# Kernel optimization log

Measured on AMD Instinct MI355X. Metric: run time of the kernel, lower is better.

Reference implementation:

```python
import jax, jax.numpy as jnp
import numpy as np
from jax import lax

H = 64      # hidden_size
VOC = 512   # num_embedding
L = 2       # num_layers


def layernorm(x, g, b, eps=1e-5):
    mu = jnp.mean(x, axis=-1, keepdims=True)
    var = jnp.mean((x - mu) ** 2, axis=-1, keepdims=True)
    return (x - mu) * lax.rsqrt(var + eps) * g + b


def conv3d(x, w, b):
    # x: [B, U, V, W, Cin] (channels-last), w: [3,3,3,Cin,Cout]
    return lax.conv_general_dilated(
        x, w, (1, 1, 1), 'SAME',
        dimension_numbers=('NDHWC', 'DHWIO', 'NDHWC')) + b


def setup_inputs() -> dict:
    key = jax.random.key(0)
    ks = jax.random.split(key, 8)
    f = lambda k, s, sc: jax.random.normal(k, s, jnp.float32) * sc
    return {
        'code': jax.random.randint(ks[0], (2, 5, 1, 8, 8, 8), 0, VOC),
        'ncode': jax.random.randint(ks[1], (2, 3, 1, 8, 8, 8), 0, VOC),
        'emb': f(ks[2], (VOC, H), 0.02),
        'win': f(ks[3], (L, 3, 3, 3, H, 4 * H), 0.05),
        'bin_': jnp.zeros((L, 4 * H), jnp.float32),
        'gin_w': jnp.ones((L, 4 * H), jnp.float32),
        'gin_b': jnp.zeros((L, 4 * H), jnp.float32),
        'wh': f(ks[4], (L, 3, 3, 3, H, 4 * H), 0.05),
        'bh': jnp.zeros((L, 4 * H), jnp.float32),
        'gh_w': jnp.ones((L, 4 * H), jnp.float32),
        'gh_b': jnp.zeros((L, 4 * H), jnp.float32),
        'w1': f(ks[5], (H, H), 0.05),
        'b1': jnp.zeros((H,), jnp.float32),
        'ln_g': jnp.ones((H,), jnp.float32),
        'ln_b': jnp.zeros((H,), jnp.float32),
        'w2': f(ks[6], (H, VOC), 0.05),
        'b2': jnp.zeros((VOC,), jnp.float32),
    }


def _forward(code, ncode, emb, win, bin_, gin_w, gin_b, wh, bh, gh_w, gh_b,
             w1, b1, ln_g, ln_b, w2, b2):
    N, Sn, C, U, V, W = ncode.shape
    x = jnp.concatenate([code, ncode[:, :-1]], axis=1)  # [N,S,C,U,V,W]
    S = x.shape[1]
    x = jnp.transpose(x, (0, 2, 1, 3, 4, 5)).reshape(N * C, S, U, V, W)
    h = emb[x]  # [NC, S, U, V, W, H]
    Hd = h.shape[-1]
    for i in range(L):
        # input-path conv is recurrence-free: batch it over all timesteps
        gi = layernorm(conv3d(h.reshape(N * C * S, U, V, W, Hd), win[i], bin_[i]),
                       gin_w[i], gin_b[i])
        gi = jnp.moveaxis(gi.reshape(N * C, S, U, V, W, 4 * Hd), 1, 0)  # [S,NC,U,V,W,4H]

        def step(carry, g, i=i):
            hx, cx = carry
            gates = g + layernorm(conv3d(hx, wh[i], bh[i]), gh_w[i], gh_b[i])
            ig, fg, cg, og = jnp.split(gates, 4, axis=-1)
            cx = jax.nn.sigmoid(fg) * cx + jax.nn.sigmoid(ig) * jnp.tanh(cg)
            hx = jax.nn.sigmoid(og) * jnp.tanh(cx)
            return (hx, cx), hx

        z = jnp.zeros((N * C, U, V, W, Hd), h.dtype)
        _, ys = lax.scan(step, (z, z), gi)
        h = jnp.moveaxis(ys, 0, 1)  # [NC,S,U,V,W,H]
    h = h[:, -Sn:].reshape(N, C, Sn, U, V, W, Hd)
    h = jnp.transpose(h, (0, 2, 1, 3, 4, 5, 6))  # [N,Sn,C,U,V,W,H]
    z = jax.nn.gelu(layernorm(h @ w1 + b1, ln_g, ln_b), approximate=False)
    logits = z @ w2 + b2  # [N,Sn,C,U,V,W,VOC]
    score = jnp.transpose(logits, (0, 6, 1, 2, 3, 4, 5))  # [N,VOC,Sn,C,U,V,W]
    logp = jax.nn.log_softmax(logits, axis=-1)
    loss = -jnp.mean(jnp.take_along_axis(logp, ncode[..., None], axis=-1))
    pred = jnp.argmax(score, axis=1)
    return score, loss, pred


def reference(code, ncode, emb, win, bin_, gin_w, gin_b, wh, bh, gh_w, gh_b,
              w1, b1, ln_g, ln_b, w2, b2):
    return _forward(code, ncode, emb, win, bin_, gin_w, gin_b, wh, bh,
                    gh_w, gh_b, w1, b1, ln_g, ln_b, w2, b2)
```

## Files before the change

### kernel.cpp

```cpp
#include <hip/hip_runtime.h>


typedef _Float16 f16;
typedef _Float16 f16x8 __attribute__((ext_vector_type(8)));
typedef float    f32x4 __attribute__((ext_vector_type(4)));

#define WSTRIDE 442368
#define WPT     884736
#define XSP     65536
#define HSP     458752

__device__ __forceinline__ float wred_sum(float v) {
    #pragma unroll
    for (int o = 32; o > 0; o >>= 1) v += __shfl_down(v, o, 64);
    return __shfl(v, 0, 64);
}
__device__ __forceinline__ float fsig(float x)  { return 1.f / (1.f + __expf(-x)); }
__device__ __forceinline__ float ftanh(float x) { return 1.f - 2.f / (__expf(2.f*x) + 1.f); }

__global__ __launch_bounds__(256) void embed_kernel(
    const int* __restrict__ code, const int* __restrict__ ncode,
    const float* __restrict__ emb, f16* __restrict__ h)
{
    int e = blockIdx.x * 256 + threadIdx.x;
    int ch = e & 63;
    int pos = e >> 6;
    int vox = pos & 511;
    int t = pos >> 9;
    int s = t % 7, nc = t / 7;
    int tok = (s < 5) ? code[(nc*5 + s)*512 + vox]
                      : ncode[(nc*3 + (s-5))*512 + vox];
    float x = emb[tok*64 + ch];
    f16 hi = (f16)x;
    h[(size_t)pos*128 + ch]      = hi;
    h[(size_t)pos*128 + 64 + ch] = (f16)(x - (float)hi);
}

__global__ __launch_bounds__(256) void wsplit_kernel(
    const float* __restrict__ win, const float* __restrict__ wh,
    f16* __restrict__ wp)
{
    int b = blockIdx.x;
    int tensor = b / 27, tap = b % 27;
    const float* src = ((tensor & 1) ? wh : win) + (tensor >> 1) * WSTRIDE
                     + tap * 16384;
    int co = threadIdx.x;
    int sw = co & 7;
    f16* dst = wp + ((size_t)(tensor*27 + tap)*256 + co) * 128;
    #pragma unroll
    for (int c8 = 0; c8 < 8; ++c8) {
        f16x8 hi8, lo8;
        #pragma unroll
        for (int j = 0; j < 8; ++j) {
            float w = src[(c8*8 + j)*256 + co] * 64.f;
            f16 hv = (f16)w;
            hi8[j] = hv;
            lo8[j] = (f16)(w - (float)hv);
        }
        *(f16x8*)(dst + ((c8 ^ sw)    )*8) = hi8;
        *(f16x8*)(dst + ((c8 ^ sw) + 8)*8) = lo8;
    }
}

struct MJob { const f16* x; const f16* w; const float* bias; float* y; };
struct MJobs { MJob j[4]; };

__global__ __launch_bounds__(256, 1) void conv_mfma_kernel(MJobs js)
{
    const MJob J = js.j[blockIdx.y];
    __shared__ float4 smem[4096];
    f16* wbuf = (f16*)smem;

    const int bx = blockIdx.x;
    const int slab = bx >> 5, u = (bx >> 2) & 7, cog = bx & 3;
    const int t = threadIdx.x, wid = t >> 6, l = t & 63;
    const int lv = (l >> 3) & 1, lw = l & 7, khi = l >> 4;

    const f16* xbase = J.x + (size_t)slab * HSP;
    const f16* wjob  = J.w + (size_t)cog * 8192;
    f16* wmine = wbuf + wid * 8192;

    const int t0 = wid * 7;
    const int ntap = (wid == 3) ? 6 : 7;

    f16x8 wreg[16];
    auto wload = [&](int tap) {
        const f16* src = wjob + (size_t)tap * 32768 + l * 8;
        #pragma unroll
        for (int i = 0; i < 16; ++i) wreg[i] = *(const f16x8*)(src + i * 512);
    };
    auto wstore = [&]() {
        f16* dst = wmine + l * 8;
        #pragma unroll
        for (int i = 0; i < 16; ++i) *(f16x8*)(dst + i * 512) = wreg[i];
    };

    wload(t0); wstore();

    f32x4 acc[4][4] = {};
    for (int tt = 0; tt < ntap; ++tt) {
        const int tap = t0 + tt;
        if (tt + 1 < ntap) wload(tap + 1);
        const int du = tap / 9, rr = tap % 9, dv = rr / 3, dw = rr % 3;
        const int uu = u + du - 1;
        const bool uok = (unsigned)uu < 8u;
        const f16* xrow[4]; bool ok[4];
        #pragma unroll
        for (int a = 0; a < 4; ++a) {
            int vs = a*2 + lv + dv - 1, ws = lw + dw - 1;
            ok[a] = uok && (unsigned)vs < 8u && (unsigned)ws < 8u;
            xrow[a] = xbase + ((size_t)(uu*64 + vs*8 + ws) << 7) + khi*8;
        }
        const f16* wrow = wmine + (l & 15) * 128;
        #pragma unroll
        for (int hs = 0; hs < 2; ++hs) {
            const int sc = ((hs*4 + khi) ^ lw) * 8;
            f16x8 ahi[4], alo[4], bhi[4], blo[4];
            #pragma unroll
            for (int a = 0; a < 4; ++a) {
                f16x8 v = {0,0,0,0,0,0,0,0}, v2 = v;
                if (ok[a]) {
                    v  = *(const f16x8*)(xrow[a] + hs*32);
                    v2 = *(const f16x8*)(xrow[a] + 64 + hs*32);
                }
                ahi[a] = v; alo[a] = v2;
            }
            #pragma unroll
            for (int n = 0; n < 4; ++n) {
                bhi[n] = *(const f16x8*)(wrow + n*2048 + sc);
                blo[n] = *(const f16x8*)(wrow + n*2048 + 64 + sc);
            }
            #pragma unroll
            for (int a = 0; a < 4; ++a)
                #pragma unroll
                for (int n = 0; n < 4; ++n)
                    acc[a][n] = __builtin_amdgcn_mfma_f32_16x16x32_f16(
                        ahi[a], bhi[n], acc[a][n], 0, 0, 0);
            #pragma unroll
            for (int a = 0; a < 4; ++a)
                #pragma unroll
                for (int n = 0; n < 4; ++n)
                    acc[a][n] = __builtin_amdgcn_mfma_f32_16x16x32_f16(
                        alo[a], bhi[n], acc[a][n], 0, 0, 0);
            #pragma unroll
            for (int a = 0; a < 4; ++a)
                #pragma unroll
                for (int n = 0; n < 4; ++n)
                    acc[a][n] = __builtin_amdgcn_mfma_f32_16x16x32_f16(
                        ahi[a], blo[n], acc[a][n], 0, 0, 0);
        }
        if (tt + 1 < ntap) wstore();
    }

    f32x4* red = (f32x4*)smem;
    {
        f32x4* mine = red + (size_t)(wid * 64 + l) * 16;
        #pragma unroll
        for (int a = 0; a < 4; ++a)
            #pragma unroll
            for (int n = 0; n < 4; ++n)
                mine[(a * 4 + n) ^ (l & 15)] = acc[a][n];
    }
    __syncthreads();
    {
        const int a = t >> 6, ll = t & 63;
        #pragma unroll
        for (int n = 0; n < 4; ++n) {
            const int ch = (a * 4 + n) ^ (ll & 15);
            f32x4 sv = red[(0 * 64 + ll) * 16 + ch]
                     + red[(1 * 64 + ll) * 16 + ch]
                     + red[(2 * 64 + ll) * 16 + ch]
                     + red[(3 * 64 + ll) * 16 + ch];
            const int co = cog * 64 + n * 16 + (ll & 15);
            const float bvv = J.bias[co];
            #pragma unroll
            for (int r = 0; r < 4; ++r) {
                int vox = a * 16 + (ll >> 4) * 4 + r;
                J.y[(size_t)(slab * 512 + u * 64 + vox) * 256 + co]
                    = sv[r] * 0.015625f + bvv;
            }
        }
    }
}

struct GJob {
    const float* giraw; const float* ghat;
    const float* ginw; const float* ginb;
    const float* ghw;  const float* ghb;
    float* cx; f16* h16; int k; int k0;
};
__global__ __launch_bounds__(256) void gates_step_kernel(GJob ja, GJob jb)
{
    const GJob J = (blockIdx.y == 0) ? ja : jb;
    const int wid = threadIdx.x >> 6, lane = threadIdx.x & 63;
    const int row = blockIdx.x * 4 + wid;
    const int nc = row >> 9, vox = row & 511;

    const float* g1 = J.giraw + (size_t)row*256;
    float a0 = g1[lane], a1 = g1[64+lane], a2 = g1[128+lane], a3 = g1[192+lane];
    float mu1 = wred_sum(a0+a1+a2+a3) * (1.f/256.f);
    float d0=a0-mu1, d1=a1-mu1, d2=a2-mu1, d3=a3-mu1;
    float v1 = wred_sum(d0*d0+d1*d1+d2*d2+d3*d3) * (1.f/256.f);
    float rs1 = rsqrtf(v1 + 1e-5f);

    const float* g2 = J.k0 ? J.ghat : J.ghat + (size_t)row*256;
    float b0 = g2[lane], b1 = g2[64+lane], b2 = g2[128+lane], b3 = g2[192+lane];
    float mu2 = wred_sum(b0+b1+b2+b3) * (1.f/256.f);
    float e0=b0-mu2, e1=b1-mu2, e2=b2-mu2, e3=b3-mu2;
    float v2 = wred_sum(e0*e0+e1*e1+e2*e2+e3*e3) * (1.f/256.f);
    float rs2 = rsqrtf(v2 + 1e-5f);

    float Ig = d0*rs1*J.ginw[lane]     + J.ginb[lane]     + e0*rs2*J.ghw[lane]     + J.ghb[lane];
    float Fg = d1*rs1*J.ginw[64+lane]  + J.ginb[64+lane]  + e1*rs2*J.ghw[64+lane]  + J.ghb[64+lane];
    float Cg = d2*rs1*J.ginw[128+lane] + J.ginb[128+lane] + e2*rs2*J.ghw[128+lane] + J.ghb[128+lane];
    float Og = d3*rs1*J.ginw[192+lane] + J.ginb[192+lane] + e3*rs2*J.ghw[192+lane] + J.ghb[192+lane];

    float c_old = J.k0 ? 0.f : J.cx[(size_t)row*64 + lane];
    float c_new = fsig(Fg)*c_old + fsig(Ig)*ftanh(Cg);
    float h_new = fsig(Og)*ftanh(c_new);
    J.cx[(size_t)row*64 + lane] = c_new;
    size_t hb = ((size_t)(nc*7 + J.k)*512 + vox)*128 + lane;
    f16 hi = (f16)h_new;
    J.h16[hb]      = hi;
    J.h16[hb + 64] = (f16)(h_new - (float)hi);
}

__global__ __launch_bounds__(256) void head_kernel(
    const f16* __restrict__ h,
    const float* __restrict__ w1, const float* __restrict__ b1,
    const float* __restrict__ lng, const float* __restrict__ lnb,
    const float* __restrict__ w2, const float* __restrict__ b2,
    const int* __restrict__ ncode,
    float* __restrict__ out)
{
    __shared__ float zv[4][64];
    __shared__ float lg[4][512];
    const int blk = blockIdx.x;
    const int n = blk / 384;
    const int sn = (blk / 128) % 3;
    const int vox0 = (blk & 127) * 4;
    const int wid = threadIdx.x >> 6, lane = threadIdx.x & 63;
    const int vox = vox0 + wid;
    const int r = (n*3 + sn)*512 + vox;
    const f16* hv = h + (size_t)((n*7 + sn + 4)*512 + vox)*128;

    float yv = b1[lane];
    for (int kk = 0; kk < 64; ++kk) {
        float hk = (float)hv[kk] + (float)hv[64 + kk];
        yv = fmaf(hk, w1[kk*64 + lane], yv);
    }
    float mu = wred_sum(yv) * (1.f/64.f);
    float d = yv - mu;
    float var = wred_sum(d*d) * (1.f/64.f);
    float ln = d * rsqrtf(var + 1e-5f) * lng[lane] + lnb[lane];
    zv[wid][lane] = 0.5f * ln * (1.f + erff(ln * 0.70710678118654752f));

    float l[8];
    #pragma unroll
    for (int j = 0; j < 8; ++j) l[j] = b2[j*64 + lane];
    for (int kk = 0; kk < 64; ++kk) {
        float zz = zv[wid][kk];
        #pragma unroll
        for (int j = 0; j < 8; ++j)
            l[j] = fmaf(zz, w2[kk*512 + j*64 + lane], l[j]);
    }
    #pragma unroll
    for (int j = 0; j < 8; ++j) lg[wid][j*64 + lane] = l[j];

    float m = l[0]; int mi = lane;
    #pragma unroll
    for (int j = 1; j < 8; ++j)
        if (l[j] > m) { m = l[j]; mi = j*64 + lane; }
    #pragma unroll
    for (int o = 32; o > 0; o >>= 1) {
        float om = __shfl_down(m, o, 64);
        int   oi = __shfl_down(mi, o, 64);
        if (om > m || (om == m && oi < mi)) { m = om; mi = oi; }
    }
    float maxv = __shfl(m, 0, 64);
    int   maxi = __shfl(mi, 0, 64);
    float es = 0.f;
    #pragma unroll
    for (int j = 0; j < 8; ++j) es += __expf(l[j] - maxv);
    float sum = wred_sum(es);
    if (lane == 0) {
        int target = ncode[(n*3 + sn)*512 + vox];
        float logp = lg[wid][target] - maxv - __logf(sum);
        atomicAdd(out + 1572864, -logp * (1.f/3072.f));
        out[1572865 + r] = (float)maxi;
    }

    __syncthreads();
    const int t = threadIdx.x;
    #pragma unroll
    for (int jj = 0; jj < 2; ++jj) {
        int co = t + jj*256;
        float4 o4 = { lg[0][co], lg[1][co], lg[2][co], lg[3][co] };
        *(float4*)(out + (size_t)((n*512 + co)*3 + sn)*512 + vox0) = o4;
    }
}

extern "C" void kernel_launch(void* const* d_in, const int* in_sizes, int n_in,
                              void* d_out, int out_size, void* d_ws, size_t ws_size,
                              hipStream_t stream) {
    (void)in_sizes; (void)n_in; (void)out_size; (void)ws_size;
    const int*   code  = (const int*)d_in[0];
    const int*   ncode = (const int*)d_in[1];
    const float* emb   = (const float*)d_in[2];
    const float* win   = (const float*)d_in[3];
    const float* bin_  = (const float*)d_in[4];
    const float* gin_w = (const float*)d_in[5];
    const float* gin_b = (const float*)d_in[6];
    const float* wh    = (const float*)d_in[7];
    const float* bh    = (const float*)d_in[8];
    const float* gh_w  = (const float*)d_in[9];
    const float* gh_b  = (const float*)d_in[10];
    const float* w1    = (const float*)d_in[11];
    const float* b1    = (const float*)d_in[12];
    const float* ln_g  = (const float*)d_in[13];
    const float* ln_b  = (const float*)d_in[14];
    const float* w2    = (const float*)d_in[15];
    const float* b2    = (const float*)d_in[16];
    float* out = (float*)d_out;

    float* base  = (float*)d_ws;
    f16*   wp    = (f16*)base;
    f16*   h1    = (f16*)(base + 1769472);
    f16*   h2    = h1 + 917504;
    float* gi1   = base + 2686976;
    float* gi2   = gi1 + 262144;
    float* ghat1 = gi2 + 262144;
    float* ghat2 = ghat1 + 262144;
    float* cx1   = ghat2 + 262144;
    float* cx2   = cx1 + 65536;

    const f16* win0 = wp;
    const f16* wh0  = wp + WPT;
    const f16* win1 = wp + 2*WPT;
    const f16* wh1  = wp + 3*WPT;

    hipMemsetAsync(out + 1572864, 0, sizeof(float), stream);
    embed_kernel<<<1792, 256, 0, stream>>>(code, ncode, emb, h1);
    wsplit_kernel<<<108, 256, 0, stream>>>(win, wh, wp);

    {
        MJobs js{};
        js.j[0] = { h1, win0, bin_, gi1 };
        conv_mfma_kernel<<<dim3(64, 1), 256, 0, stream>>>(js);
    }

    for (int s = 0; s <= 7; ++s) {
        GJob g1 = { gi1, (s == 0) ? bh : ghat1,
                    gin_w, gin_b, gh_w, gh_b, cx1, h1, s, s == 0 };
        GJob g2 = { gi2, (s == 1) ? bh + 256 : ghat2,
                    gin_w + 256, gin_b + 256, gh_w + 256, gh_b + 256,
                    cx2, h2, s - 1, s == 1 };
        if (s == 0)
            gates_step_kernel<<<dim3(256, 1), 256, 0, stream>>>(g1, g1);
        else if (s <= 6)
            gates_step_kernel<<<dim3(256, 2), 256, 0, stream>>>(g1, g2);
        else
            gates_step_kernel<<<dim3(256, 1), 256, 0, stream>>>(g2, g2);

        MJobs js{}; int nj = 0;
        if (s <= 5) js.j[nj++] = { h1 + (size_t)(s+1)*XSP, win0, bin_,     gi1 };
        if (s <= 5) js.j[nj++] = { h1 + (size_t)s*XSP,     wh0,  bh,       ghat1 };
        if (s <= 6) js.j[nj++] = { h1 + (size_t)s*XSP,     win1, bin_+256, gi2 };
        if (s >= 1 && s <= 6)
                    js.j[nj++] = { h2 + (size_t)(s-1)*XSP, wh1,  bh+256,   ghat2 };
        if (nj > 0)
            conv_mfma_kernel<<<dim3(64, nj), 256, 0, stream>>>(js);
    }

    head_kernel<<<768, 256, 0, stream>>>(h2, w1, b1, ln_g, ln_b, w2, b2, ncode, out);
}
```

Measured before the change: 335.0 us.

## Split conv K-dimension across two blocks and batch head over 16 voxels

Result: no change. 336.0 us (+0.3%).

```diff
diff --git a/kernel.cpp b/kernel.cpp
--- a/kernel.cpp
+++ b/kernel.cpp
@@ -9,6 +9,7 @@
 #define WPT     884736
 #define XSP     65536
 #define HSP     458752
+#define GPART   262144
 
 __device__ __forceinline__ float wred_sum(float v) {
     #pragma unroll
@@ -46,61 +47,67 @@
                      + tap * 16384;
     int co = threadIdx.x;
     int sw = co & 7;
-    f16* dst = wp + ((size_t)(tensor*27 + tap)*256 + co) * 128;
-    #pragma unroll
-    for (int c8 = 0; c8 < 8; ++c8) {
-        f16x8 hi8, lo8;
-        #pragma unroll
-        for (int j = 0; j < 8; ++j) {
-            float w = src[(c8*8 + j)*256 + co] * 64.f;
-            f16 hv = (f16)w;
-            hi8[j] = hv;
-            lo8[j] = (f16)(w - (float)hv);
-        }
-        *(f16x8*)(dst + ((c8 ^ sw)    )*8) = hi8;
-        *(f16x8*)(dst + ((c8 ^ sw) + 8)*8) = lo8;
-    }
-}
-
-struct MJob { const f16* x; const f16* w; const float* bias; float* y; };
+    #pragma unroll
+    for (int hs = 0; hs < 2; ++hs) {
+        f16* dst = wp + (((size_t)tensor*27 + tap)*2 + hs)*16384 + co*64;
+        #pragma unroll
+        for (int j = 0; j < 4; ++j) {
+            f16x8 hi8, lo8;
+            #pragma unroll
+            for (int m = 0; m < 8; ++m) {
+                float w = src[(hs*32 + j*8 + m)*256 + co] * 64.f;
+                f16 hv = (f16)w;
+                hi8[m] = hv;
+                lo8[m] = (f16)(w - (float)hv);
+            }
+            *(f16x8*)(dst + ((j     ^ sw))*8) = hi8;
+            *(f16x8*)(dst + (((4+j) ^ sw))*8) = lo8;
+        }
+    }
+}
+
+struct MJob { const f16* x; const f16* w; float* y; };
 struct MJobs { MJob j[4]; };
 
-__global__ __launch_bounds__(256, 1) void conv_mfma_kernel(MJobs js)
+__global__ __launch_bounds__(256, 2) void conv_mfma_kernel(MJobs js)
 {
     const MJob J = js.j[blockIdx.y];
     __shared__ float4 smem[4096];
     f16* wbuf = (f16*)smem;
 
     const int bx = blockIdx.x;
-    const int slab = bx >> 5, u = (bx >> 2) & 7, cog = bx & 3;
+    const int cog = bx & 3, u = (bx >> 2) & 7, slab = (bx >> 5) & 1, kb = bx >> 6;
     const int t = threadIdx.x, wid = t >> 6, l = t & 63;
     const int lv = (l >> 3) & 1, lw = l & 7, khi = l >> 4;
 
+    const int gid = kb*4 + wid;
+    const int g0  = (gid < 6) ? gid*7 : 42 + (gid - 6)*6;
+    const int cnt = (gid < 6) ? 7 : 6;
+
     const f16* xbase = J.x + (size_t)slab * HSP;
-    const f16* wjob  = J.w + (size_t)cog * 8192;
+    const f16* wjob  = J.w + (size_t)cog * 4096;
     f16* wmine = wbuf + wid * 8192;
 
-    const int t0 = wid * 7;
-    const int ntap = (wid == 3) ? 6 : 7;
-
-    f16x8 wreg[16];
-    auto wload = [&](int tap) {
-        const f16* src = wjob + (size_t)tap * 32768 + l * 8;
-        #pragma unroll
-        for (int i = 0; i < 16; ++i) wreg[i] = *(const f16x8*)(src + i * 512);
+    f16x8 wreg[8];
+    auto wload = [&](int k) {
+        const f16* src = wjob + (size_t)k * 16384 + l * 8;
+        #pragma unroll
+        for (int i = 0; i < 8; ++i) wreg[i] = *(const f16x8*)(src + i * 512);
     };
-    auto wstore = [&]() {
-        f16* dst = wmine + l * 8;
-        #pragma unroll
-        for (int i = 0; i < 16; ++i) *(f16x8*)(dst + i * 512) = wreg[i];
+    auto wstore = [&](int b) {
+        f16* dst = wmine + b * 4096 + l * 8;
+        #pragma unroll
+        for (int i = 0; i < 8; ++i) *(f16x8*)(dst + i * 512) = wreg[i];
     };
 
-    wload(t0); wstore();
+    wload(g0); wstore(0);
 
     f32x4 acc[4][4] = {};
-    for (int tt = 0; tt < ntap; ++tt) {
-        const int tap = t0 + tt;
-        if (tt + 1 < ntap) wload(tap + 1);
+    int cur = 0;
+    for (int q = 0; q < cnt; ++q) {
+        const int k = g0 + q;
+        if (q + 1 < cnt) wload(k + 1);
+        const int tap = k >> 1, hs = k & 1;
         const int du = tap / 9, rr = tap % 9, dv = rr / 3, dw = rr % 3;
         const int uu = u + du - 1;
         const bool uok = (unsigned)uu < 8u;
@@ -111,45 +118,43 @@
             ok[a] = uok && (unsigned)vs < 8u && (unsigned)ws < 8u;
             xrow[a] = xbase + ((size_t)(uu*64 + vs*8 + ws) << 7) + khi*8;
         }
-        const f16* wrow = wmine + (l & 15) * 128;
-        #pragma unroll
-        for (int hs = 0; hs < 2; ++hs) {
-            const int sc = ((hs*4 + khi) ^ lw) * 8;
-            f16x8 ahi[4], alo[4], bhi[4], blo[4];
-            #pragma unroll
-            for (int a = 0; a < 4; ++a) {
-                f16x8 v = {0,0,0,0,0,0,0,0}, v2 = v;
-                if (ok[a]) {
-                    v  = *(const f16x8*)(xrow[a] + hs*32);
-                    v2 = *(const f16x8*)(xrow[a] + 64 + hs*32);
-                }
-                ahi[a] = v; alo[a] = v2;
+        const f16* wrow = wmine + cur*4096 + (l & 15)*64;
+        const int schi = ((khi    ) ^ lw) * 8;
+        const int sclo = ((4 + khi) ^ lw) * 8;
+        f16x8 ahi[4], alo[4], bhi[4], blo[4];
+        #pragma unroll
+        for (int a = 0; a < 4; ++a) {
+            f16x8 v = {0,0,0,0,0,0,0,0}, v2 = v;
+            if (ok[a]) {
+                v  = *(const f16x8*)(xrow[a] + hs*32);
+                v2 = *(const f16x8*)(xrow[a] + 64 + hs*32);
             }
-            #pragma unroll
-            for (int n = 0; n < 4; ++n) {
-                bhi[n] = *(const f16x8*)(wrow + n*2048 + sc);
-                blo[n] = *(const f16x8*)(wrow + n*2048 + 64 + sc);
-            }
-            #pragma unroll
-            for (int a = 0; a < 4; ++a)
-                #pragma unroll
-                for (int n = 0; n < 4; ++n)
-                    acc[a][n] = __builtin_amdgcn_mfma_f32_16x16x32_f16(
-                        ahi[a], bhi[n], acc[a][n], 0, 0, 0);
-            #pragma unroll
-            for (int a = 0; a < 4; ++a)
-                #pragma unroll
-                for (int n = 0; n < 4; ++n)
-                    acc[a][n] = __builtin_amdgcn_mfma_f32_16x16x32_f16(
-                        alo[a], bhi[n], acc[a][n], 0, 0, 0);
-            #pragma unroll
-            for (int a = 0; a < 4; ++a)
-                #pragma unroll
-                for (int n = 0; n < 4; ++n)
-                    acc[a][n] = __builtin_amdgcn_mfma_f32_16x16x32_f16(
-                        ahi[a], blo[n], acc[a][n], 0, 0, 0);
-        }
-        if (tt + 1 < ntap) wstore();
+            ahi[a] = v; alo[a] = v2;
+        }
+        #pragma unroll
+        for (int n = 0; n < 4; ++n) {
+            bhi[n] = *(const f16x8*)(wrow + n*1024 + schi);
+            blo[n] = *(const f16x8*)(wrow + n*1024 + sclo);
+        }
+        #pragma unroll
+        for (int a = 0; a < 4; ++a)
+            #pragma unroll
+            for (int n = 0; n < 4; ++n)
+                acc[a][n] = __builtin_amdgcn_mfma_f32_16x16x32_f16(
+                    ahi[a], bhi[n], acc[a][n], 0, 0, 0);
+        #pragma unroll
+        for (int a = 0; a < 4; ++a)
+            #pragma unroll
+            for (int n = 0; n < 4; ++n)
+                acc[a][n] = __builtin_amdgcn_mfma_f32_16x16x32_f16(
+                    alo[a], bhi[n], acc[a][n], 0, 0, 0);
+        #pragma unroll
+        for (int a = 0; a < 4; ++a)
+            #pragma unroll
+            for (int n = 0; n < 4; ++n)
+                acc[a][n] = __builtin_amdgcn_mfma_f32_16x16x32_f16(
+                    ahi[a], blo[n], acc[a][n], 0, 0, 0);
+        if (q + 1 < cnt) { wstore(cur ^ 1); cur ^= 1; }
     }
 
     f32x4* red = (f32x4*)smem;
@@ -163,6 +168,7 @@
     }
     __syncthreads();
     {
+        float* yp = J.y + (size_t)kb * GPART;
         const int a = t >> 6, ll = t & 63;
         #pragma unroll
         for (int n = 0; n < 4; ++n) {
@@ -172,19 +178,20 @@
                      + red[(2 * 64 + ll) * 16 + ch]
                      + red[(3 * 64 + ll) * 16 + ch];
             const int co = cog * 64 + n * 16 + (ll & 15);
-            const float bvv = J.bias[co];
             #pragma unroll
             for (int r = 0; r < 4; ++r) {
                 int vox = a * 16 + (ll >> 4) * 4 + r;
-                J.y[(size_t)(slab * 512 + u * 64 + vox) * 256 + co]
-                    = sv[r] * 0.015625f + bvv;
+                yp[(size_t)(slab * 512 + u * 64 + vox) * 256 + co]
+                    = sv[r] * 0.015625f;
             }
         }
     }
 }
 
 struct GJob {
-    const float* giraw; const float* ghat;
+    const float* giA; const float* giB;
+    const float* ghA; const float* ghB;
+    const float* bin; const float* bhb;
     const float* ginw; const float* ginb;
     const float* ghw;  const float* ghb;
     float* cx; f16* h16; int k; int k0;
@@ -196,15 +203,29 @@
     const int row = blockIdx.x * 4 + wid;
     const int nc = row >> 9, vox = row & 511;
 
-    const float* g1 = J.giraw + (size_t)row*256;
-    float a0 = g1[lane], a1 = g1[64+lane], a2 = g1[128+lane], a3 = g1[192+lane];
+    const float* gA = J.giA + (size_t)row*256;
+    const float* gB = J.giB + (size_t)row*256;
+    float a0 = gA[lane]     + gB[lane]     + J.bin[lane];
+    float a1 = gA[64+lane]  + gB[64+lane]  + J.bin[64+lane];
+    float a2 = gA[128+lane] + gB[128+lane] + J.bin[128+lane];
+    float a3 = gA[192+lane] + gB[192+lane] + J.bin[192+lane];
     float mu1 = wred_sum(a0+a1+a2+a3) * (1.f/256.f);
     float d0=a0-mu1, d1=a1-mu1, d2=a2-mu1, d3=a3-mu1;
     float v1 = wred_sum(d0*d0+d1*d1+d2*d2+d3*d3) * (1.f/256.f);
     float rs1 = rsqrtf(v1 + 1e-5f);
 
-    const float* g2 = J.k0 ? J.ghat : J.ghat + (size_t)row*256;
-    float b0 = g2[lane], b1 = g2[64+lane], b2 = g2[128+lane], b3 = g2[192+lane];
+    float b0, b1, b2, b3;
+    if (J.k0) {
+        b0 = J.bhb[lane]; b1 = J.bhb[64+lane];
+        b2 = J.bhb[128+lane]; b3 = J.bhb[192+lane];
+    } else {
+        const float* hA = J.ghA + (size_t)row*256;
+        const float* hB = J.ghB + (size_t)row*256;
+        b0 = hA[lane]     + hB[lane]     + J.bhb[lane];
+        b1 = hA[64+lane]  + hB[64+lane]  + J.bhb[64+lane];
+        b2 = hA[128+lane] + hB[128+lane] + J.bhb[128+lane];
+        b3 = hA[192+lane] + hB[192+lane] + J.bhb[192+lane];
+    }
     float mu2 = wred_sum(b0+b1+b2+b3) * (1.f/256.f);
     float e0=b0-mu2, e1=b1-mu2, e2=b2-mu2, e3=b3-mu2;
     float v2 = wred_sum(e0*e0+e1*e1+e2*e2+e3*e3) * (1.f/256.f);
@@ -233,70 +254,99 @@
     const int* __restrict__ ncode,
     float* __restrict__ out)
 {
-    __shared__ float zv[4][64];
-    __shared__ float lg[4][512];
+    __shared__ float hsm[16][64];
+    __shared__ float zv[16][64];
+    __shared__ float lg[10240];
     const int blk = blockIdx.x;
-    const int n = blk / 384;
-    const int sn = (blk / 128) % 3;
-    const int vox0 = (blk & 127) * 4;
-    const int wid = threadIdx.x >> 6, lane = threadIdx.x & 63;
-    const int vox = vox0 + wid;
-    const int r = (n*3 + sn)*512 + vox;
-    const f16* hv = h + (size_t)((n*7 + sn + 4)*512 + vox)*128;
-
-    float yv = b1[lane];
+    const int n = blk / 96;
+    const int sn = (blk / 32) % 3;
+    const int vox0 = (blk & 31) * 16;
+    const int t = threadIdx.x, wid = t >> 6, lane = t & 63;
+
+    for (int idx = t; idx < 1024; idx += 256) {
+        int vr = idx >> 6, ch = idx & 63;
+        const f16* hv = h + (size_t)((n*7 + sn + 4)*512 + vox0 + vr)*128;
+        hsm[vr][ch] = (float)hv[ch] + (float)hv[64 + ch];
+    }
+    __syncthreads();
+
+    float yva[4], yvb[4];
+    #pragma unroll
+    for (int r = 0; r < 4; ++r) { yva[r] = b1[lane]; yvb[r] = 0.f; }
+    for (int kk = 0; kk < 64; kk += 2) {
+        float w1a = w1[kk*64 + lane], w1b = w1[(kk+1)*64 + lane];
+        #pragma unroll
+        for (int r = 0; r < 4; ++r) {
+            yva[r] = fmaf(hsm[wid*4 + r][kk],     w1a, yva[r]);
+            yvb[r] = fmaf(hsm[wid*4 + r][kk + 1], w1b, yvb[r]);
+        }
+    }
+    #pragma unroll
+    for (int r = 0; r < 4; ++r) {
+        float yv = yva[r] + yvb[r];
+        float mu = wred_sum(yv) * (1.f/64.f);
+        float d = yv - mu;
+        float var = wred_sum(d*d) * (1.f/64.f);
+        float ln = d * rsqrtf(var + 1e-5f) * lng[lane] + lnb[lane];
+        zv[wid*4 + r][lane] = 0.5f * ln * (1.f + erff(ln * 0.70710678118654752f));
+    }
+    __syncthreads();
+
+    float l[4][8];
+    #pragma unroll
+    for (int r = 0; r < 4; ++r)
+        #pragma unroll
+        for (int j = 0; j < 8; ++j) l[r][j] = b2[j*64 + lane];
     for (int kk = 0; kk < 64; ++kk) {
-        float hk = (float)hv[kk] + (float)hv[64 + kk];
-        yv = fmaf(hk, w1[kk*64 + lane], yv);
-    }
-    float mu = wred_sum(yv) * (1.f/64.f);
-    float d = yv - mu;
-    float var = wred_sum(d*d) * (1.f/64.f);
-    float ln = d * rsqrtf(var + 1e-5f) * lng[lane] + lnb[lane];
-    zv[wid][lane] = 0.5f * ln * (1.f + erff(ln * 0.70710678118654752f));
-
-    float l[8];
-    #pragma unroll
-    for (int j = 0; j < 8; ++j) l[j] = b2[j*64 + lane];
-    for (int kk = 0; kk < 64; ++kk) {
-        float zz = zv[wid][kk];
+        float wv[8];
+        #pragma unroll
+        for (int j = 0; j < 8; ++j) wv[j] = w2[kk*512 + j*64 + lane];
+        #pragma unroll
+        for (int r = 0; r < 4; ++r) {
+            float zz = zv[wid*4 + r][kk];
+            #pragma unroll
+            for (int j = 0; j < 8; ++j) l[r][j] = fmaf(zz, wv[j], l[r][j]);
+        }
+    }
+    #pragma unroll
+    for (int r = 0; r < 4; ++r)
         #pragma unroll
         for (int j = 0; j < 8; ++j)
-            l[j] = fmaf(zz, w2[kk*512 + j*64 + lane], l[j]);
-    }
-    #pragma unroll
-    for (int j = 0; j < 8; ++j) lg[wid][j*64 + lane] = l[j];
-
-    float m = l[0]; int mi = lane;
-    #pragma unroll
-    for (int j = 1; j < 8; ++j)
-        if (l[j] > m) { m = l[j]; mi = j*64 + lane; }
-    #pragma unroll
-    for (int o = 32; o > 0; o >>= 1) {
-        float om = __shfl_down(m, o, 64);
-        int   oi = __shfl_down(mi, o, 64);
-        if (om > m || (om == m && oi < mi)) { m = om; mi = oi; }
-    }
-    float maxv = __shfl(m, 0, 64);
-    int   maxi = __shfl(mi, 0, 64);
-    float es = 0.f;
-    #pragma unroll
-    for (int j = 0; j < 8; ++j) es += __expf(l[j] - maxv);
-    float sum = wred_sum(es);
-    if (lane == 0) {
-        int target = ncode[(n*3 + sn)*512 + vox];
-        float logp = lg[wid][target] - maxv - __logf(sum);
-        atomicAdd(out + 1572864, -logp * (1.f/3072.f));
-        out[1572865 + r] = (float)maxi;
+            lg[(j*64 + lane)*20 + wid*4 + r] = l[r][j];
+
+    #pragma unroll
+    for (int r = 0; r < 4; ++r) {
+        float m = l[r][0]; int mi = lane;
+        #pragma unroll
+        for (int j = 1; j < 8; ++j)
+            if (l[r][j] > m) { m = l[r][j]; mi = j*64 + lane; }
+        #pragma unroll
+        for (int o = 32; o > 0; o >>= 1) {
+            float om = __shfl_down(m, o, 64);
+            int   oi = __shfl_down(mi, o, 64);
+            if (om > m || (om == m && oi < mi)) { m = om; mi = oi; }
+        }
+        float maxv = __shfl(m, 0, 64);
+        int   maxi = __shfl(mi, 0, 64);
+        float es = 0.f;
+        #pragma unroll
+        for (int j = 0; j < 8; ++j) es += __expf(l[r][j] - maxv);
+        float sum = wred_sum(es);
+        if (lane == 0) {
+            int vox = vox0 + wid*4 + r;
+            int target = ncode[(n*3 + sn)*512 + vox];
+            float logp = lg[target*20 + wid*4 + r] - maxv - __logf(sum);
+            atomicAdd(out + 1572864, -logp * (1.f/3072.f));
+            out[1572865 + (n*3 + sn)*512 + vox] = (float)maxi;
+        }
     }
 
     __syncthreads();
-    const int t = threadIdx.x;
-    #pragma unroll
-    for (int jj = 0; jj < 2; ++jj) {
-        int co = t + jj*256;
-        float4 o4 = { lg[0][co], lg[1][co], lg[2][co], lg[3][co] };
-        *(float4*)(out + (size_t)((n*512 + co)*3 + sn)*512 + vox0) = o4;
+    for (int e = t; e < 2048; e += 256) {
+        int co = e >> 2, p = e & 3;
+        int base = co*20 + p*4;
+        float4 o4 = { lg[base], lg[base+1], lg[base+2], lg[base+3] };
+        *(float4*)(out + (size_t)((n*512 + co)*3 + sn)*512 + vox0 + p*4) = o4;
     }
 }
 
@@ -328,10 +378,10 @@
     f16*   h1    = (f16*)(base + 1769472);
     f16*   h2    = h1 + 917504;
     float* gi1   = base + 2686976;
-    float* gi2   = gi1 + 262144;
-    float* ghat1 = gi2 + 262144;
-    float* ghat2 = ghat1 + 262144;
-    float* cx1   = ghat2 + 262144;
+    float* gi2   = gi1 + 2*GPART;
+    float* ghat1 = gi2 + 2*GPART;
+    float* ghat2 = ghat1 + 2*GPART;
+    float* cx1   = ghat2 + 2*GPART;
     float* cx2   = cx1 + 65536;
 
     const f16* win0 = wp;
@@ -345,14 +395,14 @@
 
     {
         MJobs js{};
-        js.j[0] = { h1, win0, bin_, gi1 };
-        conv_mfma_kernel<<<dim3(64, 1), 256, 0, stream>>>(js);
+        js.j[0] = { h1, win0, gi1 };
+        conv_mfma_kernel<<<dim3(128, 1), 256, 0, stream>>>(js);
     }
 
     for (int s = 0; s <= 7; ++s) {
-        GJob g1 = { gi1, (s == 0) ? bh : ghat1,
+        GJob g1 = { gi1, gi1 + GPART, ghat1, ghat1 + GPART, bin_, bh,
                     gin_w, gin_b, gh_w, gh_b, cx1, h1, s, s == 0 };
-        GJob g2 = { gi2, (s == 1) ? bh + 256 : ghat2,
+        GJob g2 = { gi2, gi2 + GPART, ghat2, ghat2 + GPART, bin_ + 256, bh + 256,
                     gin_w + 256, gin_b + 256, gh_w + 256, gh_b + 256,
                     cx2, h2, s - 1, s == 1 };
         if (s == 0)
@@ -363,14 +413,14 @@
             gates_step_kernel<<<dim3(256, 1), 256, 0, stream>>>(g2, g2);
 
         MJobs js{}; int nj = 0;
-        if (s <= 5) js.j[nj++] = { h1 + (size_t)(s+1)*XSP, win0, bin_,     gi1 };
-        if (s <= 5) js.j[nj++] = { h1 + (size_t)s*XSP,     wh0,  bh,       ghat1 };
-        if (s <= 6) js.j[nj++] = { h1 + (size_t)s*XSP,     win1, bin_+256, gi2 };
+        if (s <= 5) js.j[nj++] = { h1 + (size_t)(s+1)*XSP, win0, gi1 };
+        if (s <= 5) js.j[nj++] = { h1 + (size_t)s*XSP,     wh0,  ghat1 };
+        if (s <= 6) js.j[nj++] = { h1 + (size_t)s*XSP,     win1, gi2 };
         if (s >= 1 && s <= 6)
-                    js.j[nj++] = { h2 + (size_t)(s-1)*XSP, wh1,  bh+256,   ghat2 };
+                    js.j[nj++] = { h2 + (size_t)(s-1)*XSP, wh1,  ghat2 };
         if (nj > 0)
-            conv_mfma_kernel<<<dim3(64, nj), 256, 0, stream>>>(js);
-    }
-
-    head_kernel<<<768, 256, 0, stream>>>(h2, w1, b1, ln_g, ln_b, w2, b2, ncode, out);
-}
+            conv_mfma_kernel<<<dim3(128, nj), 256, 0, stream>>>(js);
+    }
+
+    head_kernel<<<192, 256, 0, stream>>>(h2, w1, b1, ln_g, ln_b, w2, b2, ncode, out);
+}
```
